# Optimization experiments

Measured on AMD Instinct MI355X. Metric: run time of the kernel, lower is better.

## Reference

```python
import jax, jax.numpy as jnp
import numpy as np

B, L, C_IN, C_OUTER, C_OUT = 1, 768, 384, 32, 128
EPS = 1e-5


def setup_inputs() -> dict:
    key = jax.random.key(0)
    ks = jax.random.split(key, 4)
    return {
        "act": jax.random.normal(ks[0], (B, L, C_IN), dtype=jnp.float32),
        "mask": jnp.ones((B, L), dtype=jnp.float32),
        "norm_w": jnp.ones((C_IN,), dtype=jnp.float32),
        "norm_b": jnp.zeros((C_IN,), dtype=jnp.float32),
        "wl": jax.random.normal(ks[1], (C_IN, C_OUTER), dtype=jnp.float32) * 0.05,
        "bl": jnp.zeros((C_OUTER,), dtype=jnp.float32),
        "wr": jax.random.normal(ks[2], (C_IN, C_OUTER), dtype=jnp.float32) * 0.05,
        "br": jnp.zeros((C_OUTER,), dtype=jnp.float32),
        "wo": jax.random.normal(ks[3], (2 * C_OUTER, C_OUT), dtype=jnp.float32) * 0.05,
        "bo": jnp.zeros((C_OUT,), dtype=jnp.float32),
    }


def reference(act, mask, norm_w, norm_b, wl, bl, wr, br, wo, bo):
    # LayerNorm over channel dim
    mu = jnp.mean(act, axis=-1, keepdims=True)
    var = jnp.mean(jnp.square(act - mu), axis=-1, keepdims=True)
    normed = (act - mu) * jax.lax.rsqrt(var + EPS) * norm_w + norm_b

    m = mask[..., None]  # (b, l, 1)
    left = m * (jnp.einsum('blc,cd->bld', normed, wl) + bl)   # (b, l, d)
    right = m * (jnp.einsum('blc,cd->bld', normed, wr) + br)  # (b, l, d)

    # pairwise: index j from left, index i from right (matches torch broadcasting)
    prod = left[:, None, :, :] * right[:, :, None, :]  # (b, i, j, d)
    diff = left[:, None, :, :] - right[:, :, None, :]  # (b, i, j, d)
    pair = jnp.concatenate([prod, diff], axis=-1)      # (b, i, j, 2d)
    return jnp.einsum('bijd,de->bije', pair, wo) + bo  # (b, l, l, c_out)
```

## Files before the change

kernel.cpp:

```cpp
#include <hip/hip_runtime.h>

#define LSEQ 768
#define CIN 384
#define DOUT 32
#define EOUT 128
#define EPS 1e-5f
#define JT 96

__global__ __launch_bounds__(384) void k_ln_proj(
    const float* __restrict__ act, const float* __restrict__ mask,
    const float* __restrict__ nw, const float* __restrict__ nb,
    const float* __restrict__ wl, const float* __restrict__ bl,
    const float* __restrict__ wr, const float* __restrict__ br,
    const float* __restrict__ wo,
    float* __restrict__ left, float* __restrict__ right,
    float* __restrict__ l2, float* __restrict__ r2)
{
    const int row = blockIdx.x;
    const int t = threadIdx.x;
    __shared__ float red[6];
    __shared__ float norm_s[CIN];
    __shared__ float part[64][6];
    __shared__ float lr_s[64];

    float a = act[row * CIN + t];

    float v = a;
    #pragma unroll
    for (int off = 32; off; off >>= 1) v += __shfl_down(v, off, 64);
    const int wave = t >> 6;
    if ((t & 63) == 0) red[wave] = v;
    __syncthreads();
    float mu = (red[0] + red[1] + red[2] + red[3] + red[4] + red[5]) * (1.0f / CIN);

    float d = a - mu;
    v = d * d;
    #pragma unroll
    for (int off = 32; off; off >>= 1) v += __shfl_down(v, off, 64);
    __syncthreads();
    if ((t & 63) == 0) red[wave] = v;
    __syncthreads();
    float var = (red[0] + red[1] + red[2] + red[3] + red[4] + red[5]) * (1.0f / CIN);
    float rstd = rsqrtf(var + EPS);

    norm_s[t] = d * rstd * nw[t] + nb[t];
    __syncthreads();

    const int dd = t & 63;
    const int chunk = t >> 6;
    const float* __restrict__ w = (dd < DOUT) ? wl : wr;
    const int dcol = dd & (DOUT - 1);
    const int c0 = chunk * 64;
    float p = 0.f;
    #pragma unroll 8
    for (int c = 0; c < 64; ++c)
        p = fmaf(norm_s[c0 + c], w[(c0 + c) * DOUT + dcol], p);
    part[dd][chunk] = p;
    __syncthreads();

    if (t < 64) {
        float s = part[t][0] + part[t][1] + part[t][2] + part[t][3] + part[t][4] + part[t][5];
        float bias = (t < DOUT) ? bl[t] : br[t - DOUT];
        float val = (s + bias) * mask[row];
        lr_s[t] = val;
        if (t < DOUT) left[row * DOUT + t] = val;
        else          right[row * DOUT + (t - DOUT)] = val;
    }
    __syncthreads();

    if (t < 256) {
        const int e = t & (EOUT - 1);
        const bool isR = (t >= EOUT);
        const float* __restrict__ lr = isR ? (lr_s + DOUT) : lr_s;
        float acc = 0.f;
        #pragma unroll
        for (int dq = 0; dq < DOUT; ++dq)
            acc = fmaf(lr[dq], wo[(DOUT + dq) * EOUT + e], acc);
        (isR ? r2 : l2)[row * EOUT + e] = acc;
    }
}

__global__ __launch_bounds__(128) void k_outer(
    const float* __restrict__ left, const float* __restrict__ right,
    const float* __restrict__ l2, const float* __restrict__ r2,
    const float* __restrict__ wo, const float* __restrict__ bo,
    float* __restrict__ out)
{
    const int i = blockIdx.x;
    const int j0 = blockIdx.y * JT;
    const int e = threadIdx.x;

    const float* __restrict__ Rrow = right + i * DOUT;
    float wi[DOUT];
    #pragma unroll
    for (int d = 0; d < DOUT; ++d)
        wi[d] = Rrow[d] * wo[d * EOUT + e];

    const float base = bo[e] - r2[i * EOUT + e];
    const float* __restrict__ l2p = l2 + (size_t)j0 * EOUT + e;
    float* __restrict__ op = out + ((size_t)i * LSEQ + j0) * EOUT + e;

    #pragma unroll 2
    for (int j = 0; j < JT; ++j) {
        const float* __restrict__ Lrow = left + (size_t)(j0 + j) * DOUT;
        float acc = base;
        #pragma unroll
        for (int d = 0; d < DOUT; ++d)
            acc = fmaf(Lrow[d], wi[d], acc);
        acc += l2p[(size_t)j * EOUT];
        op[(size_t)j * EOUT] = acc;
    }
}

extern "C" void kernel_launch(void* const* d_in, const int* in_sizes, int n_in,
                              void* d_out, int out_size, void* d_ws, size_t ws_size,
                              hipStream_t stream) {
    const float* act  = (const float*)d_in[0];
    const float* mask = (const float*)d_in[1];
    const float* nw   = (const float*)d_in[2];
    const float* nb   = (const float*)d_in[3];
    const float* wl   = (const float*)d_in[4];
    const float* bl   = (const float*)d_in[5];
    const float* wr   = (const float*)d_in[6];
    const float* br   = (const float*)d_in[7];
    const float* wo   = (const float*)d_in[8];
    const float* bo   = (const float*)d_in[9];
    float* out = (float*)d_out;

    float* ws    = (float*)d_ws;
    float* left  = ws;
    float* right = ws + LSEQ * DOUT;
    float* l2    = ws + 2 * LSEQ * DOUT;
    float* r2    = l2 + LSEQ * EOUT;

    hipLaunchKernelGGL(k_ln_proj, dim3(LSEQ), dim3(384), 0, stream,
                       act, mask, nw, nb, wl, bl, wr, br, wo,
                       left, right, l2, r2);
    hipLaunchKernelGGL(k_outer, dim3(LSEQ, LSEQ / JT), dim3(128), 0, stream,
                       left, right, l2, r2, wo, bo, out);
}
```

Baseline: 395.7 us.

## Compute pairwise outer projection with bf16 MFMA instead of scalar FMAs

Stores left projections as bf16 and replaces the per-thread 32-term FMA loop with a 16x16x32 bf16 MFMA per 16-row tile, one block of 8 waves per i covering all 128 output channels and all j. This moves the contraction onto matrix cores and drops the j-tiling grid dimension. It lowers precision of the left and right-times-wo operands to bf16, which adds rounding error, and the kernel stays bound by writing the large fp32 output.

```diff
diff --git a/kernel.cpp b/kernel.cpp
--- a/kernel.cpp
+++ b/kernel.cpp
@@ -1,11 +1,14 @@
 #include <hip/hip_runtime.h>
+#include <hip/hip_bf16.h>
 
 #define LSEQ 768
 #define CIN 384
 #define DOUT 32
 #define EOUT 128
 #define EPS 1e-5f
-#define JT 96
+
+typedef __attribute__((ext_vector_type(8))) short bf16x8;
+typedef __attribute__((ext_vector_type(4))) float f32x4;
 
 __global__ __launch_bounds__(384) void k_ln_proj(
     const float* __restrict__ act, const float* __restrict__ mask,
@@ -13,7 +16,7 @@
     const float* __restrict__ wl, const float* __restrict__ bl,
     const float* __restrict__ wr, const float* __restrict__ br,
     const float* __restrict__ wo,
-    float* __restrict__ left, float* __restrict__ right,
+    __hip_bfloat16* __restrict__ left_bf, float* __restrict__ right,
     float* __restrict__ l2, float* __restrict__ r2)
 {
     const int row = blockIdx.x;
@@ -63,7 +66,7 @@
         float bias = (t < DOUT) ? bl[t] : br[t - DOUT];
         float val = (s + bias) * mask[row];
         lr_s[t] = val;
-        if (t < DOUT) left[row * DOUT + t] = val;
+        if (t < DOUT) left_bf[row * DOUT + t] = __float2bfloat16(val);
         else          right[row * DOUT + (t - DOUT)] = val;
     }
     __syncthreads();
@@ -80,35 +83,45 @@
     }
 }
 
-__global__ __launch_bounds__(128) void k_outer(
-    const float* __restrict__ left, const float* __restrict__ right,
+__global__ __launch_bounds__(512) void k_outer_mfma(
+    const __hip_bfloat16* __restrict__ left_bf,
+    const float* __restrict__ right,
     const float* __restrict__ l2, const float* __restrict__ r2,
     const float* __restrict__ wo, const float* __restrict__ bo,
     float* __restrict__ out)
 {
     const int i = blockIdx.x;
-    const int j0 = blockIdx.y * JT;
-    const int e = threadIdx.x;
+    const int t = threadIdx.x;
+    const int lane = t & 63;
+    const int wv = t >> 6;
+    const int n = lane & 15;
+    const int g = lane >> 4;
+    const int e = wv * 16 + n;
 
+    bf16x8 bfrag;
     const float* __restrict__ Rrow = right + i * DOUT;
-    float wi[DOUT];
     #pragma unroll
-    for (int d = 0; d < DOUT; ++d)
-        wi[d] = Rrow[d] * wo[d * EOUT + e];
+    for (int q = 0; q < 8; ++q) {
+        const int k = 8 * g + q;
+        const float v = Rrow[k] * wo[k * EOUT + e];
+        __hip_bfloat16 h = __float2bfloat16(v);
+        bfrag[q] = *reinterpret_cast<const short*>(&h);
+    }
+    const float rb = bo[e] - r2[i * EOUT + e];
 
-    const float base = bo[e] - r2[i * EOUT + e];
-    const float* __restrict__ l2p = l2 + (size_t)j0 * EOUT + e;
-    float* __restrict__ op = out + ((size_t)i * LSEQ + j0) * EOUT + e;
+    const f32x4 zero = {0.f, 0.f, 0.f, 0.f};
+    float* __restrict__ op = out + (size_t)i * LSEQ * EOUT;
+    const short* __restrict__ lbf = reinterpret_cast<const short*>(left_bf);
 
     #pragma unroll 2
-    for (int j = 0; j < JT; ++j) {
-        const float* __restrict__ Lrow = left + (size_t)(j0 + j) * DOUT;
-        float acc = base;
+    for (int jt = 0; jt < LSEQ / 16; ++jt) {
+        const bf16x8 afr = *reinterpret_cast<const bf16x8*>(lbf + (jt * 16 + n) * DOUT + 8 * g);
+        const f32x4 dfr = __builtin_amdgcn_mfma_f32_16x16x32_bf16(afr, bfrag, zero, 0, 0, 0);
+        const int j = jt * 16 + 4 * g;
         #pragma unroll
-        for (int d = 0; d < DOUT; ++d)
-            acc = fmaf(Lrow[d], wi[d], acc);
-        acc += l2p[(size_t)j * EOUT];
-        op[(size_t)j * EOUT] = acc;
+        for (int q = 0; q < 4; ++q) {
+            op[(size_t)(j + q) * EOUT + e] = dfr[q] + l2[(j + q) * EOUT + e] + rb;
+        }
     }
 }
 
@@ -127,15 +140,15 @@
     const float* bo   = (const float*)d_in[9];
     float* out = (float*)d_out;
 
-    float* ws    = (float*)d_ws;
-    float* left  = ws;
-    float* right = ws + LSEQ * DOUT;
-    float* l2    = ws + 2 * LSEQ * DOUT;
-    float* r2    = l2 + LSEQ * EOUT;
+    char* ws = (char*)d_ws;
+    __hip_bfloat16* left_bf = (__hip_bfloat16*)(ws);
+    float* right = (float*)(ws + 49152);
+    float* l2    = (float*)(ws + 49152 + 98304);
+    float* r2    = (float*)(ws + 49152 + 98304 + 393216);
 
     hipLaunchKernelGGL(k_ln_proj, dim3(LSEQ), dim3(384), 0, stream,
                        act, mask, nw, nb, wl, bl, wr, br, wo,
-                       left, right, l2, r2);
-    hipLaunchKernelGGL(k_outer, dim3(LSEQ, LSEQ / JT), dim3(128), 0, stream,
-                       left, right, l2, r2, wo, bo, out);
+                       left_bf, right, l2, r2);
+    hipLaunchKernelGGL(k_outer_mfma, dim3(LSEQ), dim3(512), 0, stream,
+                       left_bf, right, l2, r2, wo, bo, out);
 }
```

Result: faster. 363.5 us (-8.1%).
